# Kernel tuning notes

Measured on AMD Instinct MI355X. Metric: run time of the kernel, lower is better.

The kernel has to match this reference:

```python
import jax, jax.numpy as jnp
import numpy as np

N_NODES = 100000
N_EDGES = 3200000
D_FEAT = 512


def setup_inputs() -> dict:
    key = jax.random.key(0)
    k1, k2, k3, k4 = jax.random.split(key, 4)
    x = jax.random.normal(k1, (N_NODES, D_FEAT), dtype=jnp.float32)
    edge_index = jax.random.randint(k2, (2, N_EDGES), 0, N_NODES, dtype=jnp.int64)
    # Glorot-ish init for GCN layer weights
    W1 = jax.random.normal(k3, (D_FEAT, 16), dtype=jnp.float32) * (1.0 / np.sqrt(D_FEAT))
    b1 = jnp.zeros((16,), dtype=jnp.float32)
    W2 = jax.random.normal(k4, (16, 2), dtype=jnp.float32) * (1.0 / np.sqrt(16))
    b2 = jnp.zeros((2,), dtype=jnp.float32)
    return {"x": x, "edge_index": edge_index, "W1": W1, "b1": b1, "W2": W2, "b2": b2}


def _gcn_prep(edge_index, n_nodes):
    # add self-loops and compute symmetric normalization (GCNConv default)
    row = jnp.concatenate([edge_index[0], jnp.arange(n_nodes, dtype=edge_index.dtype)])
    col = jnp.concatenate([edge_index[1], jnp.arange(n_nodes, dtype=edge_index.dtype)])
    deg = jax.ops.segment_sum(jnp.ones_like(row, dtype=jnp.float32), row,
                              num_segments=n_nodes)
    deg_isqrt = jnp.where(deg > 0, jax.lax.rsqrt(deg), 0.0)
    norm = deg_isqrt[row] * deg_isqrt[col]  # [E+N]
    return row, col, norm


def _gcn_conv(x, W, b, row, col, norm, n_nodes):
    h = x @ W                              # [N, out]
    msg = h[col] * norm[:, None]           # gather + scale  [E+N, out]
    out = jax.ops.segment_sum(msg, row, num_segments=n_nodes)  # scatter-add
    return out + b


def reference(x, edge_index, W1, b1, W2, b2):
    n_nodes = x.shape[0]
    row, col, norm = _gcn_prep(edge_index, n_nodes)
    h = _gcn_conv(x, W1, b1, row, col, norm, n_nodes)
    h = jax.nn.relu(h)
    # dropout is identity in eval mode (deterministic reference)
    h = _gcn_conv(h, W2, b2, row, col, norm, n_nodes)
    return jax.nn.log_softmax(h, axis=1)
```

## Files before the change

kernel.cpp:

```cpp
#include <hip/hip_runtime.h>
#include <math.h>


#define DF 512
#define H1F 16
#define BROWS 256
#define PA_VPT 16
#define PA_BATCH 4096
#define A2_CAP 10240

typedef short bf16x8 __attribute__((ext_vector_type(8)));
typedef float f32x4 __attribute__((ext_vector_type(4)));
typedef _Float16 half8 __attribute__((ext_vector_type(8)));
typedef unsigned int u32x4 __attribute__((ext_vector_type(4)));

static __device__ __forceinline__ short bf16_rne(float f) {
    unsigned int u = __builtin_bit_cast(unsigned int, f);
    unsigned int r = (u + 0x7FFFu + ((u >> 16) & 1u)) >> 16;
    return (short)r;
}
static __device__ __forceinline__ unsigned int cvt_pk_bf16(float lo, float hi) {
    unsigned int r;
    asm("v_cvt_pk_bf16_f32 %0, %1, %2" : "=v"(r) : "v"(lo), "v"(hi));
    return r;
}

__global__ __launch_bounds__(256) void k_hist(const int* __restrict__ rowi,
                                              unsigned int* __restrict__ ghist,
                                              int E, int nbkt, int nblkp) {
    __shared__ unsigned int hist[512];
    int t = threadIdx.x;
    hist[t] = 0u; hist[t + 256] = 0u;
    __syncthreads();
    int base = blockIdx.x * PA_BATCH;
    int ne = E - base; if (ne > PA_BATCH) ne = PA_BATCH;
    if (ne == PA_BATCH) {
        const int4* p4 = (const int4*)(rowi + base);
#pragma unroll
        for (int j = 0; j < 4; ++j) {
            int4 v = p4[j * 256 + t];
            atomicAdd(&hist[(unsigned int)v.x >> 8], 1u);
            atomicAdd(&hist[(unsigned int)v.y >> 8], 1u);
            atomicAdd(&hist[(unsigned int)v.z >> 8], 1u);
            atomicAdd(&hist[(unsigned int)v.w >> 8], 1u);
        }
    } else {
        for (int j = t; j < ne; j += 256)
            atomicAdd(&hist[(unsigned int)rowi[base + j] >> 8], 1u);
    }
    __syncthreads();
    for (int b = t; b < nbkt; b += 256)
        ghist[(size_t)b * nblkp + blockIdx.x] = hist[b];
}

__global__ __launch_bounds__(256) void k_colscan(const unsigned int* __restrict__ ghist,
                                                 unsigned int* __restrict__ gbase,
                                                 unsigned int* __restrict__ btot,
                                                 int nblk, int nblkp) {
    __shared__ unsigned int s[256];
    int t = threadIdx.x, b = blockIdx.x;
    unsigned int carry = 0u;
    int nch = (nblk + 255) / 256;
    for (int ch = 0; ch < nch; ++ch) {
        int idx = ch * 256 + t;
        unsigned int v = (idx < nblk) ? ghist[(size_t)b * nblkp + idx] : 0u;
        s[t] = v;
        __syncthreads();
        for (int off = 1; off < 256; off <<= 1) {
            unsigned int u = (t >= off) ? s[t - off] : 0u;
            __syncthreads();
            s[t] += u;
            __syncthreads();
        }
        if (idx < nblk) gbase[(size_t)b * nblkp + idx] = carry + s[t] - v;
        unsigned int tot = s[255];
        __syncthreads();
        carry += tot;
    }
    if (t == 0) btot[b] = carry;
}

__global__ __launch_bounds__(256) void k_scatter(const int* __restrict__ rowi,
                                                 const int* __restrict__ coli,
                                                 const unsigned int* __restrict__ gbase,
                                                 const unsigned int* __restrict__ btot,
                                                 unsigned int* __restrict__ pairs,
                                                 int E, int nbkt, int nblkp) {
    __shared__ unsigned int hist[512];
    __shared__ unsigned int sA[512];
    __shared__ unsigned int sB[512];
    __shared__ unsigned int gb[512];
    __shared__ unsigned int reorder[PA_BATCH];
    __shared__ unsigned short bid[PA_BATCH];
    int t = threadIdx.x;
    int base = blockIdx.x * PA_BATCH;
    int ne = E - base; if (ne > PA_BATCH) ne = PA_BATCH;

    unsigned int b0 = (t < nbkt) ? btot[t] : 0u;
    unsigned int b1v = (t + 256 < nbkt) ? btot[t + 256] : 0u;
    sA[t] = b0; sA[t + 256] = b1v;
    __syncthreads();
    {
        unsigned int* src = sA; unsigned int* dst = sB;
        for (int off = 1; off < 512; off <<= 1) {
            unsigned int v0 = src[t] + ((t >= off) ? src[t - off] : 0u);
            unsigned int v1 = src[t + 256] + src[t + 256 - off];
            dst[t] = v0; dst[t + 256] = v1;
            __syncthreads();
            unsigned int* tmp = src; src = dst; dst = tmp;
        }
        gb[t] = src[t] - b0;
        gb[t + 256] = src[t + 256] - b1v;
        if (t < nbkt) gb[t] += gbase[(size_t)t * nblkp + blockIdx.x];
        if (t + 256 < nbkt) gb[t + 256] += gbase[(size_t)(t + 256) * nblkp + blockIdx.x];
    }

    hist[t] = 0u; hist[t + 256] = 0u;
    __syncthreads();

    unsigned int pk[PA_VPT]; unsigned int bk[PA_VPT]; unsigned int rk[PA_VPT];
    if (ne == PA_BATCH) {
        const int4* r4 = (const int4*)(rowi + base);
        const int4* c4 = (const int4*)(coli + base);
#pragma unroll
        for (int jj = 0; jj < 4; ++jj) {
            int4 rv = r4[jj * 256 + t];
            int4 cv = c4[jj * 256 + t];
            int rr[4] = {rv.x, rv.y, rv.z, rv.w};
            int cc[4] = {cv.x, cv.y, cv.z, cv.w};
#pragma unroll
            for (int q = 0; q < 4; ++q) {
                int j = jj * 4 + q;
                unsigned int b = (unsigned int)rr[q] >> 8;
                pk[j] = ((unsigned int)(rr[q] & (BROWS - 1)) << 17) | (unsigned int)cc[q];
                bk[j] = b;
                rk[j] = atomicAdd(&hist[b], 1u);
            }
        }
    } else {
#pragma unroll
        for (int j = 0; j < PA_VPT; ++j) {
            int idx = j * 256 + t;
            if (idx < ne) {
                int r = rowi[base + idx];
                int c = coli[base + idx];
                unsigned int b = (unsigned int)r >> 8;
                pk[j] = ((unsigned int)(r & (BROWS - 1)) << 17) | (unsigned int)c;
                bk[j] = b;
                rk[j] = atomicAdd(&hist[b], 1u);
            } else bk[j] = 0xFFFFFFFFu;
        }
    }
    __syncthreads();

    sA[t] = hist[t]; sA[t + 256] = hist[t + 256];
    __syncthreads();
    unsigned int* src = sA; unsigned int* dst = sB;
    for (int off = 1; off < 512; off <<= 1) {
        unsigned int v0 = src[t] + ((t >= off) ? src[t - off] : 0u);
        unsigned int v1 = src[t + 256] + src[t + 256 - off];
        dst[t] = v0; dst[t + 256] = v1;
        __syncthreads();
        unsigned int* tmp = src; src = dst; dst = tmp;
    }

#pragma unroll
    for (int j = 0; j < PA_VPT; ++j) {
        if ((ne == PA_BATCH) || (bk[j] != 0xFFFFFFFFu)) {
            unsigned int b = bk[j];
            unsigned int slot = src[b] - hist[b] + rk[j];
            reorder[slot] = pk[j];
            bid[slot] = (unsigned short)b;
        }
    }
    __syncthreads();

    for (int s = t; s < ne; s += 256) {
        unsigned int b = bid[s];
        unsigned int off = src[b] - hist[b];
        pairs[gb[b] + ((unsigned int)s - off)] = reorder[s];
    }
}

__global__ __launch_bounds__(512) void k_count(const unsigned int* __restrict__ pairs,
                                               const unsigned int* __restrict__ btot,
                                               unsigned int* __restrict__ bpref_g,
                                               unsigned int* __restrict__ rowloc,
                                               float* __restrict__ isq, int n, int nbkt) {
    __shared__ unsigned int bsc[512];
    __shared__ unsigned int rcnt[256];
    __shared__ unsigned int ssc[256];
    int t = threadIdx.x;
    int b = blockIdx.x;
    int r0 = b * 256;

    bsc[t] = (t < nbkt) ? btot[t] : 0u;
    __syncthreads();
    for (int off = 1; off < 512; off <<= 1) {
        unsigned int u = (t >= off) ? bsc[t - off] : 0u;
        __syncthreads();
        bsc[t] += u;
        __syncthreads();
    }
    unsigned int bp = (b > 0) ? bsc[b - 1] : 0u;
    unsigned int cnt = btot[b];
    if (t == 0) bpref_g[b] = bp;
    if (cnt > A2_CAP) cnt = A2_CAP;

    if (t < 256) rcnt[t] = 0u;
    __syncthreads();
    {
        unsigned int nv4 = cnt >> 2;
        const u32x4* p4 = (const u32x4*)(pairs + bp);
        for (unsigned int i = t; i < nv4; i += 512) {
            u32x4 v = p4[i];
            atomicAdd(&rcnt[v[0] >> 17], 1u);
            atomicAdd(&rcnt[v[1] >> 17], 1u);
            atomicAdd(&rcnt[v[2] >> 17], 1u);
            atomicAdd(&rcnt[v[3] >> 17], 1u);
        }
        for (unsigned int i = (nv4 << 2) + t; i < cnt; i += 512)
            atomicAdd(&rcnt[pairs[bp + i] >> 17], 1u);
    }
    __syncthreads();
    unsigned int d = 0;
    if (t < 256) { d = rcnt[t]; ssc[t] = d; }
    __syncthreads();
    for (int off = 1; off < 256; off <<= 1) {
        unsigned int u = 0;
        if (t < 256 && t >= off) u = ssc[t - off];
        __syncthreads();
        if (t < 256) ssc[t] += u;
        __syncthreads();
    }
    if (t < 256 && r0 + t < n) {
        rowloc[r0 + t] = ssc[t] - d;
        isq[r0 + t] = rsqrtf((float)(d + 1u));
    }
}

__global__ __launch_bounds__(256) void k_gemm1(const float* __restrict__ x,
                                               const float* __restrict__ W1,
                                               const float* __restrict__ isq,
                                               _Float16* __restrict__ h1h,
                                               int n, int ntile, int tstride) {
    int wave = threadIdx.x >> 6;
    int lane = threadIdx.x & 63;
    int g = lane >> 4;
    int m = lane & 15;

    bf16x8 wf[16];
#pragma unroll
    for (int s = 0; s < 16; ++s) {
#pragma unroll
        for (int j = 0; j < 8; ++j) {
            int k = s * 32 + g * 8 + j;
            wf[s][j] = bf16_rne(W1[k * H1F + m]);
        }
    }

    for (int tile = blockIdx.x * 4 + wave; tile < ntile; tile += tstride) {
        long r0 = (long)tile * 16;
        const float* xrow = x + (r0 + m) * DF;
        f32x4 acc = {0.0f, 0.0f, 0.0f, 0.0f};
#pragma unroll
        for (int s = 0; s < 16; ++s) {
            const float4* p = (const float4*)(xrow + s * 32 + g * 8);
            float4 a0 = p[0];
            float4 a1 = p[1];
            u32x4 aw;
            aw[0] = cvt_pk_bf16(a0.x, a0.y);
            aw[1] = cvt_pk_bf16(a0.z, a0.w);
            aw[2] = cvt_pk_bf16(a1.x, a1.y);
            aw[3] = cvt_pk_bf16(a1.z, a1.w);
            bf16x8 af = __builtin_bit_cast(bf16x8, aw);
            acc = __builtin_amdgcn_mfma_f32_16x16x32_bf16(af, wf[s], acc, 0, 0, 0);
        }
#pragma unroll
        for (int j = 0; j < 4; ++j) {
            long rr = r0 + g * 4 + j;
            h1h[rr * H1F + m] = (_Float16)(isq[rr] * acc[j]);
        }
    }
}

__global__ __launch_bounds__(1024) void k_sortg1(const unsigned int* __restrict__ pairs,
                                                 const unsigned int* __restrict__ btot,
                                                 const unsigned int* __restrict__ bpref_g,
                                                 const unsigned int* __restrict__ rowloc,
                                                 const float* __restrict__ isq,
                                                 const _Float16* __restrict__ h1h,
                                                 const float* __restrict__ b1,
                                                 _Float16* __restrict__ r1h, int n) {
    __shared__ unsigned int sorted[A2_CAP];
    __shared__ unsigned int rloc[256];
    __shared__ unsigned int rcur[256];
    int t = threadIdx.x;
    int b = blockIdx.x;
    int r0 = b * 256;
    unsigned int bp = bpref_g[b];
    unsigned int cnt = btot[b];
    if (cnt > A2_CAP) cnt = A2_CAP;

    if (t < 256) {
        rloc[t] = (r0 + t < n) ? rowloc[r0 + t] : 0u;
        rcur[t] = 0u;
    }
    __syncthreads();
    for (unsigned int i = t; i < cnt; i += 1024) {
        unsigned int p = pairs[bp + i];
        unsigned int lr = p >> 17;
        unsigned int rk = atomicAdd(&rcur[lr], 1u);
        sorted[rloc[lr] + rk] = p & 0x1FFFFu;
    }
    __syncthreads();

    int lr = t >> 2;
    int r = r0 + lr;
    if (r >= n) return;
    int hf = t & 1, sg = (t >> 1) & 1;
    unsigned int start = rloc[lr];
    unsigned int cntr = rcur[lr];
    float s = isq[r];
    const half8* hb = (const half8*)h1h;
    float acc[8];
    if (sg == 0) {
        half8 me = hb[(size_t)r * 2 + hf];
#pragma unroll
        for (int i = 0; i < 8; ++i) acc[i] = (float)me[i];
    } else {
#pragma unroll
        for (int i = 0; i < 8; ++i) acc[i] = 0.0f;
    }
    unsigned int k = sg;
    for (; k + 2 < cntr; k += 4) {
        unsigned int c0 = sorted[start + k];
        unsigned int c1 = sorted[start + k + 2];
        half8 v0 = hb[(size_t)c0 * 2 + hf];
        half8 v1 = hb[(size_t)c1 * 2 + hf];
#pragma unroll
        for (int i = 0; i < 8; ++i) acc[i] += (float)v0[i] + (float)v1[i];
    }
    for (; k < cntr; k += 2) {
        unsigned int c0 = sorted[start + k];
        half8 v0 = hb[(size_t)c0 * 2 + hf];
#pragma unroll
        for (int i = 0; i < 8; ++i) acc[i] += (float)v0[i];
    }
#pragma unroll
    for (int i = 0; i < 8; ++i) acc[i] += __shfl_xor(acc[i], 2);
    if (sg == 0) {
        const float* b1p = b1 + hf * 8;
        half8 o;
#pragma unroll
        for (int i = 0; i < 8; ++i)
            o[i] = (_Float16)(s * fmaxf(fmaf(s, acc[i], b1p[i]), 0.0f));
        ((half8*)r1h)[(size_t)r * 2 + hf] = o;
    }
}

__global__ __launch_bounds__(1024) void k_sortg2(const unsigned int* __restrict__ pairs,
                                                 const unsigned int* __restrict__ btot,
                                                 const unsigned int* __restrict__ bpref_g,
                                                 const unsigned int* __restrict__ rowloc,
                                                 const float* __restrict__ isq,
                                                 const _Float16* __restrict__ r1h,
                                                 const float* __restrict__ W2,
                                                 const float* __restrict__ b2,
                                                 float* __restrict__ out, int n) {
    __shared__ unsigned int sorted[A2_CAP];
    __shared__ unsigned int rloc[256];
    __shared__ unsigned int rcur[256];
    int t = threadIdx.x;
    int b = blockIdx.x;
    int r0 = b * 256;
    unsigned int bp = bpref_g[b];
    unsigned int cnt = btot[b];
    if (cnt > A2_CAP) cnt = A2_CAP;

    if (t < 256) {
        rloc[t] = (r0 + t < n) ? rowloc[r0 + t] : 0u;
        rcur[t] = 0u;
    }
    __syncthreads();
    for (unsigned int i = t; i < cnt; i += 1024) {
        unsigned int p = pairs[bp + i];
        unsigned int lr = p >> 17;
        unsigned int rk = atomicAdd(&rcur[lr], 1u);
        sorted[rloc[lr] + rk] = p & 0x1FFFFu;
    }
    __syncthreads();

    int lr = t >> 2;
    int r = r0 + lr;
    if (r >= n) return;
    int hf = t & 1, sg = (t >> 1) & 1;
    unsigned int start = rloc[lr];
    unsigned int cntr = rcur[lr];
    float s = isq[r];
    const half8* hb = (const half8*)r1h;
    float acc[8];
    if (sg == 0) {
        half8 me = hb[(size_t)r * 2 + hf];
#pragma unroll
        for (int i = 0; i < 8; ++i) acc[i] = (float)me[i];
    } else {
#pragma unroll
        for (int i = 0; i < 8; ++i) acc[i] = 0.0f;
    }
    unsigned int k = sg;
    for (; k + 2 < cntr; k += 4) {
        unsigned int c0 = sorted[start + k];
        unsigned int c1 = sorted[start + k + 2];
        half8 v0 = hb[(size_t)c0 * 2 + hf];
        half8 v1 = hb[(size_t)c1 * 2 + hf];
#pragma unroll
        for (int i = 0; i < 8; ++i) acc[i] += (float)v0[i] + (float)v1[i];
    }
    for (; k < cntr; k += 2) {
        unsigned int c0 = sorted[start + k];
        half8 v0 = hb[(size_t)c0 * 2 + hf];
#pragma unroll
        for (int i = 0; i < 8; ++i) acc[i] += (float)v0[i];
    }
#pragma unroll
    for (int i = 0; i < 8; ++i) acc[i] += __shfl_xor(acc[i], 2);
    int f0 = hf * 8;
    float o0 = 0.0f, o1 = 0.0f;
#pragma unroll
    for (int i = 0; i < 8; ++i) {
        o0 = fmaf(acc[i], W2[(f0 + i) * 2 + 0], o0);
        o1 = fmaf(acc[i], W2[(f0 + i) * 2 + 1], o1);
    }
    o0 += __shfl_xor(o0, 1);
    o1 += __shfl_xor(o1, 1);
    if ((t & 3) == 0) {
        float a = fmaf(s, o0, b2[0]);
        float bb = fmaf(s, o1, b2[1]);
        float m = fmaxf(a, bb);
        float lse = m + logf(expf(a - m) + expf(bb - m));
        out[(size_t)r * 2 + 0] = a - lse;
        out[(size_t)r * 2 + 1] = bb - lse;
    }
}

extern "C" void kernel_launch(void* const* d_in, const int* in_sizes, int n_in,
                              void* d_out, int out_size, void* d_ws, size_t ws_size,
                              hipStream_t stream) {
    const float* x  = (const float*)d_in[0];
    const int*   ei = (const int*)d_in[1];
    const float* W1 = (const float*)d_in[2];
    const float* b1 = (const float*)d_in[3];
    const float* W2 = (const float*)d_in[4];
    const float* b2 = (const float*)d_in[5];

    int n = in_sizes[0] / DF;
    int E = in_sizes[1] / 2;
    const int* rowi = ei;
    const int* coli = ei + E;

    int NBKT = (n + BROWS - 1) / BROWS;
    int NBLK = (E + PA_BATCH - 1) / PA_BATCH;
    int NBLKP = NBLK + 2;

    char* base = (char*)d_ws;
    float*        isq    = (float*)base;        base += (size_t)n * 4;
    unsigned int* rowloc = (unsigned int*)base; base += (size_t)n * 4;
    unsigned int* btot   = (unsigned int*)base; base += 512 * 4;
    unsigned int* bpref  = (unsigned int*)base; base += 512 * 4;
    unsigned int* ghist  = (unsigned int*)base; base += (size_t)NBKT * NBLKP * 4;
    unsigned int* gbase  = (unsigned int*)base; base += (size_t)NBKT * NBLKP * 4;
    _Float16*     h1h    = (_Float16*)base;     base += (size_t)n * H1F * 2;
    _Float16*     r1h    = (_Float16*)base;     base += (size_t)n * H1F * 2;
    unsigned int* pairs  = (unsigned int*)base; base += (size_t)E * 4;
    float*        out    = (float*)d_out;

    k_hist<<<NBLK, 256, 0, stream>>>(rowi, ghist, E, NBKT, NBLKP);
    k_colscan<<<NBKT, 256, 0, stream>>>(ghist, gbase, btot, NBLK, NBLKP);
    k_scatter<<<NBLK, 256, 0, stream>>>(rowi, coli, gbase, btot, pairs, E, NBKT, NBLKP);
    k_count<<<NBKT, 512, 0, stream>>>(pairs, btot, bpref, rowloc, isq, n, NBKT);
    {
        int ntile = (n + 15) / 16;
        int ngrid = 782;
        k_gemm1<<<ngrid, 256, 0, stream>>>(x, W1, isq, h1h, n, ntile, ngrid * 4);
    }
    k_sortg1<<<NBKT, 1024, 0, stream>>>(pairs, btot, bpref, rowloc, isq, h1h, b1, r1h, n);
    k_sortg2<<<NBKT, 1024, 0, stream>>>(pairs, btot, bpref, rowloc, isq, r1h, W2, b2, out, n);
}
```

Baseline: 125.7 us.

## Reuse layer-1 sorted edge lists in layer 2 and widen gather unroll

The first aggregation kernel now writes its per-block sorted neighbor list back into the pairs buffer. The second kernel can then copy it straight into shared memory instead of redoing the atomic counting sort, and it derives per-row counts from rowloc prefix offsets. Pair loads now use 128-bit vector reads, and the neighbor gather loop is unrolled to four outstanding loads per thread to raise memory-level parallelism. The price is an extra global write of the sorted list in layer 1 and a new dependency on pairs being mutated between the two kernels.

```diff
diff --git a/kernel.cpp b/kernel.cpp
--- a/kernel.cpp
+++ b/kernel.cpp
@@ -284,7 +284,7 @@
     }
 }
 
-__global__ __launch_bounds__(1024) void k_sortg1(const unsigned int* __restrict__ pairs,
+__global__ __launch_bounds__(1024) void k_sortg1(unsigned int* __restrict__ pairs,
                                                  const unsigned int* __restrict__ btot,
                                                  const unsigned int* __restrict__ bpref_g,
                                                  const unsigned int* __restrict__ rowloc,
@@ -307,13 +307,27 @@
         rcur[t] = 0u;
     }
     __syncthreads();
-    for (unsigned int i = t; i < cnt; i += 1024) {
-        unsigned int p = pairs[bp + i];
-        unsigned int lr = p >> 17;
-        unsigned int rk = atomicAdd(&rcur[lr], 1u);
-        sorted[rloc[lr] + rk] = p & 0x1FFFFu;
-    }
-    __syncthreads();
+    {
+        unsigned int nv4 = cnt >> 2;
+        const u32x4* p4 = (const u32x4*)(pairs + bp);
+        for (unsigned int i = t; i < nv4; i += 1024) {
+            u32x4 v = p4[i];
+#pragma unroll
+            for (int q = 0; q < 4; ++q) {
+                unsigned int lr = v[q] >> 17;
+                unsigned int rk = atomicAdd(&rcur[lr], 1u);
+                sorted[rloc[lr] + rk] = v[q] & 0x1FFFFu;
+            }
+        }
+        for (unsigned int i = (nv4 << 2) + t; i < cnt; i += 1024) {
+            unsigned int p = pairs[bp + i];
+            unsigned int lr = p >> 17;
+            unsigned int rk = atomicAdd(&rcur[lr], 1u);
+            sorted[rloc[lr] + rk] = p & 0x1FFFFu;
+        }
+    }
+    __syncthreads();
+    for (unsigned int i = t; i < cnt; i += 1024) pairs[bp + i] = sorted[i];
 
     int lr = t >> 2;
     int r = r0 + lr;
@@ -333,13 +347,18 @@
         for (int i = 0; i < 8; ++i) acc[i] = 0.0f;
     }
     unsigned int k = sg;
-    for (; k + 2 < cntr; k += 4) {
+    for (; k + 6 < cntr; k += 8) {
         unsigned int c0 = sorted[start + k];
         unsigned int c1 = sorted[start + k + 2];
+        unsigned int c2 = sorted[start + k + 4];
+        unsigned int c3 = sorted[start + k + 6];
         half8 v0 = hb[(size_t)c0 * 2 + hf];
         half8 v1 = hb[(size_t)c1 * 2 + hf];
-#pragma unroll
-        for (int i = 0; i < 8; ++i) acc[i] += (float)v0[i] + (float)v1[i];
+        half8 v2 = hb[(size_t)c2 * 2 + hf];
+        half8 v3 = hb[(size_t)c3 * 2 + hf];
+#pragma unroll
+        for (int i = 0; i < 8; ++i)
+            acc[i] += ((float)v0[i] + (float)v1[i]) + ((float)v2[i] + (float)v3[i]);
     }
     for (; k < cntr; k += 2) {
         unsigned int c0 = sorted[start + k];
@@ -369,8 +388,7 @@
                                                  const float* __restrict__ b2,
                                                  float* __restrict__ out, int n) {
     __shared__ unsigned int sorted[A2_CAP];
-    __shared__ unsigned int rloc[256];
-    __shared__ unsigned int rcur[256];
+    __shared__ unsigned int rloc[257];
     int t = threadIdx.x;
     int b = blockIdx.x;
     int r0 = b * 256;
@@ -378,16 +396,22 @@
     unsigned int cnt = btot[b];
     if (cnt > A2_CAP) cnt = A2_CAP;
 
-    if (t < 256) {
-        rloc[t] = (r0 + t < n) ? rowloc[r0 + t] : 0u;
-        rcur[t] = 0u;
-    }
-    __syncthreads();
-    for (unsigned int i = t; i < cnt; i += 1024) {
-        unsigned int p = pairs[bp + i];
-        unsigned int lr = p >> 17;
-        unsigned int rk = atomicAdd(&rcur[lr], 1u);
-        sorted[rloc[lr] + rk] = p & 0x1FFFFu;
+    if (t < 256) rloc[t] = (r0 + t < n) ? rowloc[r0 + t] : cnt;
+    if (t == 0) rloc[256] = cnt;
+    __syncthreads();
+    {
+        unsigned int nv4 = cnt >> 2;
+        const u32x4* p4 = (const u32x4*)(pairs + bp);
+        for (unsigned int i = t; i < nv4; i += 1024) {
+            u32x4 v = p4[i];
+            unsigned int j = i << 2;
+            sorted[j + 0] = v[0];
+            sorted[j + 1] = v[1];
+            sorted[j + 2] = v[2];
+            sorted[j + 3] = v[3];
+        }
+        for (unsigned int i = (nv4 << 2) + t; i < cnt; i += 1024)
+            sorted[i] = pairs[bp + i];
     }
     __syncthreads();
 
@@ -396,7 +420,7 @@
     if (r >= n) return;
     int hf = t & 1, sg = (t >> 1) & 1;
     unsigned int start = rloc[lr];
-    unsigned int cntr = rcur[lr];
+    unsigned int cntr = rloc[lr + 1] - start;
     float s = isq[r];
     const half8* hb = (const half8*)r1h;
     float acc[8];
@@ -409,13 +433,18 @@
         for (int i = 0; i < 8; ++i) acc[i] = 0.0f;
     }
     unsigned int k = sg;
-    for (; k + 2 < cntr; k += 4) {
+    for (; k + 6 < cntr; k += 8) {
         unsigned int c0 = sorted[start + k];
         unsigned int c1 = sorted[start + k + 2];
+        unsigned int c2 = sorted[start + k + 4];
+        unsigned int c3 = sorted[start + k + 6];
         half8 v0 = hb[(size_t)c0 * 2 + hf];
         half8 v1 = hb[(size_t)c1 * 2 + hf];
-#pragma unroll
-        for (int i = 0; i < 8; ++i) acc[i] += (float)v0[i] + (float)v1[i];
+        half8 v2 = hb[(size_t)c2 * 2 + hf];
+        half8 v3 = hb[(size_t)c3 * 2 + hf];
+#pragma unroll
+        for (int i = 0; i < 8; ++i)
+            acc[i] += ((float)v0[i] + (float)v1[i]) + ((float)v2[i] + (float)v3[i]);
     }
     for (; k < cntr; k += 2) {
         unsigned int c0 = sorted[start + k];
```

Result: slower. 130.3 us (+3.6%).
